# Kernel optimization log

Measured on AMD Instinct MI355X. Metric: run time of the kernel, lower is better.

Reference implementation:

```python
import jax, jax.numpy as jnp
import numpy as np

E = 16        # n_routed_experts
K = 4         # num_experts_per_tok
G = 4         # n_group
TG = 2        # topk_group
NS = 2        # n_shared_experts
H = 1024      # hidden_size
I = 1408      # intermediate_size
SCALE = 1.0   # routed_scaling_factor


def _gate(x2d, gate_w, gate_bias):
    # x2d: [T,H], gate_w: [E,H], gate_bias: [E]
    T = x2d.shape[0]
    logits = x2d.astype(jnp.float32) @ gate_w.astype(jnp.float32).T   # [T,E]
    scores = jax.nn.sigmoid(logits)
    sfc = scores + gate_bias[None, :]
    # group scores = sum of top-2 expert scores within each group
    grp = sfc.reshape(T, G, E // G)
    top2, _ = jax.lax.top_k(grp, 2)
    group_scores = top2.sum(-1)                                       # [T,G]
    _, gidx = jax.lax.top_k(group_scores, TG)                         # [T,TG]
    gmask = jnp.zeros((T, G), sfc.dtype).at[jnp.arange(T)[:, None], gidx].set(1.0)
    smask = jnp.repeat(gmask, E // G, axis=1) > 0                     # [T,E]
    tmp = jnp.where(smask, sfc, 0.0)
    _, topk_idx = jax.lax.top_k(tmp, K)                               # [T,K]
    topk_w = jnp.take_along_axis(scores, topk_idx, axis=1)            # [T,K]
    topk_w = topk_w / (topk_w.sum(-1, keepdims=True) + 1e-20)         # norm_topk_prob
    return topk_idx, topk_w * SCALE


def setup_inputs() -> dict:
    key = jax.random.key(0)
    ks = jax.random.split(key, 8)
    bound = 1.0 / np.sqrt(H)  # kaiming_uniform(a=sqrt(5)) on [E,H]
    return {
        "hidden_states": jax.random.normal(ks[0], (1, 1024, H), jnp.float32),
        "gate_w": jax.random.uniform(ks[1], (E, H), jnp.float32, -bound, bound),
        "gate_bias": jnp.zeros((E,), jnp.float32),
        "gate_proj": jax.random.normal(ks[2], (E, I, H), jnp.float32) * 0.02,
        "up_proj": jax.random.normal(ks[3], (E, I, H), jnp.float32) * 0.02,
        "down_proj": jax.random.normal(ks[4], (E, H, I), jnp.float32) * 0.02,
        "shared_gate_w": jax.random.normal(ks[5], (I * NS, H), jnp.float32) * 0.02,
        "shared_up_w": jax.random.normal(ks[6], (I * NS, H), jnp.float32) * 0.02,
        "shared_down_w": jax.random.normal(ks[7], (H, I * NS), jnp.float32) * 0.02,
    }


def reference(hidden_states, gate_w, gate_bias, gate_proj, up_proj, down_proj,
              shared_gate_w, shared_up_w, shared_down_w):
    orig_shape = hidden_states.shape
    x = hidden_states.reshape(-1, H)                                  # [T,H]
    topk_idx, topk_w = _gate(x, gate_w, gate_bias)
    # per-token per-expert combine weight (top-k indices are unique per token,
    # so scatter-add combine == dense weighted sum)
    combine_w = (jax.nn.one_hot(topk_idx, E, dtype=x.dtype) * topk_w[..., None]).sum(1)  # [T,E]
    g = jnp.einsum('th,eih->tei', x, gate_proj)                       # [T,E,I]
    u = jnp.einsum('th,eih->tei', x, up_proj)
    act = jax.nn.silu(g) * u                                          # SwiGLU
    y = jnp.einsum('tei,ehi,te->th', act, down_proj, combine_w)       # [T,H]
    # shared experts
    sg = x @ shared_gate_w.T
    su = x @ shared_up_w.T
    y = y + (jax.nn.silu(sg) * su) @ shared_down_w.T
    return y.reshape(orig_shape)
```

## Files before the change

### kernel.cpp

```cpp
#include <hip/hip_runtime.h>
#include <hip/hip_bf16.h>

#define T_TOK 1024
#define H_DIM 1024
#define I_DIM 1408
#define NE 16
#define NEP 18
#define BM 256

typedef __attribute__((ext_vector_type(8))) __bf16 bf16x8;
typedef __attribute__((ext_vector_type(4))) float f32x4;

__device__ __forceinline__ bf16x8 cvt8(float4 a, float4 b) {
    bf16x8 r;
    r[0] = (__bf16)a.x; r[1] = (__bf16)a.y; r[2] = (__bf16)a.z; r[3] = (__bf16)a.w;
    r[4] = (__bf16)b.x; r[5] = (__bf16)b.y; r[6] = (__bf16)b.z; r[7] = (__bf16)b.w;
    return r;
}

__device__ __forceinline__ void gll16(const float* g, float* l) {
    __builtin_amdgcn_global_load_lds(
        (const __attribute__((address_space(1))) void*)g,
        (__attribute__((address_space(3))) void*)l, 16, 0, 0);
}

__global__ __launch_bounds__(64) void gate_kernel(
    const float* __restrict__ x, const float* __restrict__ gw,
    const float* __restrict__ gb,
    int* __restrict__ counts, int* __restrict__ etok, float* __restrict__ ew)
{
    const int t = blockIdx.x;
    const int lane = threadIdx.x;
    float s[NE];
#pragma unroll
    for (int e = 0; e < NE; ++e) s[e] = 0.f;
    const float* xr = x + (size_t)t * H_DIM;
    for (int i = lane; i < H_DIM; i += 64) {
        float xv = xr[i];
#pragma unroll
        for (int e = 0; e < NE; ++e) s[e] += xv * gw[e * H_DIM + i];
    }
#pragma unroll
    for (int e = 0; e < NE; ++e) {
        for (int off = 32; off > 0; off >>= 1) s[e] += __shfl_xor(s[e], off);
    }
    if (lane == 0) {
        float scores[NE], sfc[NE];
#pragma unroll
        for (int e = 0; e < NE; ++e) {
            scores[e] = 1.f / (1.f + __expf(-s[e]));
            sfc[e] = scores[e] + gb[e];
        }
        float gsc[4];
#pragma unroll
        for (int g = 0; g < 4; ++g) {
            float m1 = -1e30f, m2 = -1e30f;
#pragma unroll
            for (int j = 0; j < 4; ++j) {
                float v = sfc[4 * g + j];
                if (v > m1) { m2 = m1; m1 = v; } else if (v > m2) { m2 = v; }
            }
            gsc[g] = m1 + m2;
        }
        int g1 = 0;
        for (int g = 1; g < 4; ++g) if (gsc[g] > gsc[g1]) g1 = g;
        int g2 = -1;
        for (int g = 0; g < 4; ++g) {
            if (g == g1) continue;
            if (g2 < 0 || gsc[g] > gsc[g2]) g2 = g;
        }
        float tmp[NE];
#pragma unroll
        for (int e = 0; e < NE; ++e) {
            int gg = e >> 2;
            tmp[e] = (gg == g1 || gg == g2) ? sfc[e] : 0.0f;
        }
        int idxs[4]; float wk[4]; float wsum = 0.f;
#pragma unroll
        for (int k = 0; k < 4; ++k) {
            int bi = 0;
            for (int e = 1; e < NE; ++e) if (tmp[e] > tmp[bi]) bi = e;
            idxs[k] = bi; wk[k] = scores[bi]; wsum += scores[bi];
            tmp[bi] = -1e30f;
        }
        float inv = 1.f / (wsum + 1e-20f);
        for (int k = 0; k < 4; ++k) {
            int e = idxs[k];
            int pos = atomicAdd(&counts[e], 1);
            etok[e * T_TOK + pos] = t;
            ew[e * T_TOK + pos] = wk[k] * inv;
        }
    }
}

__global__ __launch_bounds__(256) void cvtx_kernel(
    const float* __restrict__ x, __hip_bfloat16* __restrict__ x_bf)
{
    int i = (blockIdx.x * 256 + threadIdx.x) * 4;
    float4 v = ((const float4*)x)[i >> 2];
    x_bf[i + 0] = __float2bfloat16(v.x);
    x_bf[i + 1] = __float2bfloat16(v.y);
    x_bf[i + 2] = __float2bfloat16(v.z);
    x_bf[i + 3] = __float2bfloat16(v.w);
}

__global__ __launch_bounds__(256, 2) void gateup_kernel(
    const __hip_bfloat16* __restrict__ x_bf,
    const float* __restrict__ gproj, const float* __restrict__ uproj,
    const float* __restrict__ sgw, const float* __restrict__ suw,
    const int* __restrict__ counts, const int* __restrict__ etok,
    __hip_bfloat16* __restrict__ act, int e0)
{
    const int slot = blockIdx.y;
    const int e = e0 + slot;
    const int cnt = (e < NE) ? counts[e] : T_TOK;
    const int row0 = blockIdx.z * BM;
    if (row0 >= cnt) return;

    __shared__ int toks[BM];
    __shared__ __align__(16) float Bg[3][2048];
    __shared__ __align__(16) float Bu[3][2048];

    const int tid = threadIdx.x;
    {
        int r = row0 + tid;
        toks[tid] = (e < NE) ? ((r < cnt) ? etok[e * T_TOK + r] : 0) : r;
    }

    const int nb0 = blockIdx.x * 64;
    const float *wg, *wu;
    if (e < NE) {
        wg = gproj + (size_t)e * I_DIM * H_DIM;
        wu = uproj + (size_t)e * I_DIM * H_DIM;
    } else {
        wg = sgw + (size_t)(e - NE) * I_DIM * H_DIM;
        wu = suw + (size_t)(e - NE) * I_DIM * H_DIM;
    }

    const int lane = tid & 63;
    const int w = tid >> 6;
    const int col = lane & 15, kq = lane >> 4;

    const int lr8 = lane >> 3;
    const int sgx = (lane & 7) ^ lr8;
    const float* pgW[2]; const float* puW[2];
#pragma unroll
    for (int j = 0; j < 2; ++j) {
        int c = 2 * w + j;
        pgW[j] = wg + (size_t)(nb0 + c * 8 + lr8) * H_DIM + sgx * 4;
        puW[j] = wu + (size_t)(nb0 + c * 8 + lr8) * H_DIM + sgx * 4;
    }
    const int ldsw0 = (2 * w) * 256, ldsw1 = (2 * w + 1) * 256;

    int offs[4][2];
#pragma unroll
    for (int ni = 0; ni < 4; ++ni) {
        int row = ni * 16 + col;
#pragma unroll
        for (int h = 0; h < 2; ++h)
            offs[ni][h] = row * 32 + (((kq * 2 + h) ^ (row & 7)) << 2);
    }

    __syncthreads();

    const __hip_bfloat16* ar[4];
#pragma unroll
    for (int mi = 0; mi < 4; ++mi)
        ar[mi] = x_bf + (size_t)toks[w * 64 + mi * 16 + col] * H_DIM + kq * 8;

    f32x4 accg[4][4], accu[4][4];
#pragma unroll
    for (int mi = 0; mi < 4; ++mi)
#pragma unroll
        for (int ni = 0; ni < 4; ++ni) {
            accg[mi][ni] = (f32x4){0.f, 0.f, 0.f, 0.f};
            accu[mi][ni] = (f32x4){0.f, 0.f, 0.f, 0.f};
        }

    bf16x8 a_cur[4], a_nxt[4];
#pragma unroll
    for (int mi = 0; mi < 4; ++mi) a_cur[mi] = *(const bf16x8*)ar[mi];
    gll16(pgW[0], &Bg[0][ldsw0]); gll16(pgW[1], &Bg[0][ldsw1]);
    gll16(puW[0], &Bu[0][ldsw0]); gll16(puW[1], &Bu[0][ldsw1]);
    gll16(pgW[0] + 32, &Bg[1][ldsw0]); gll16(pgW[1] + 32, &Bg[1][ldsw1]);
    gll16(puW[0] + 32, &Bu[1][ldsw0]); gll16(puW[1] + 32, &Bu[1][ldsw1]);

    int br = 0;
    for (int k = 0; k < 32; ++k) {
        asm volatile("s_waitcnt vmcnt(4)" ::: "memory");
        __builtin_amdgcn_s_barrier();
        __builtin_amdgcn_sched_barrier(0);
        if (k + 1 < 32) {
#pragma unroll
            for (int mi = 0; mi < 4; ++mi)
                a_nxt[mi] = *(const bf16x8*)(ar[mi] + (k + 1) * 32);
        }
        __builtin_amdgcn_sched_barrier(0);
        if (k + 2 < 32) {
            int b2 = br + 2; if (b2 >= 3) b2 -= 3;
            float* bgD = &Bg[0][0] + b2 * 2048;
            float* buD = &Bu[0][0] + b2 * 2048;
            const int ko = (k + 2) * 32;
            gll16(pgW[0] + ko, bgD + ldsw0); gll16(pgW[1] + ko, bgD + ldsw1);
            gll16(puW[0] + ko, buD + ldsw0); gll16(puW[1] + ko, buD + ldsw1);
        }
        __builtin_amdgcn_sched_barrier(0);
        const float* bgR = &Bg[0][0] + br * 2048;
        const float* buR = &Bu[0][0] + br * 2048;
        bf16x8 bg[4], bu[4];
#pragma unroll
        for (int ni = 0; ni < 4; ++ni) {
            float4 lo = *(const float4*)(bgR + offs[ni][0]);
            float4 hi = *(const float4*)(bgR + offs[ni][1]);
            bg[ni] = cvt8(lo, hi);
            float4 lo2 = *(const float4*)(buR + offs[ni][0]);
            float4 hi2 = *(const float4*)(buR + offs[ni][1]);
            bu[ni] = cvt8(lo2, hi2);
        }
#pragma unroll
        for (int mi = 0; mi < 4; ++mi)
#pragma unroll
            for (int ni = 0; ni < 4; ++ni) {
                accg[mi][ni] = __builtin_amdgcn_mfma_f32_16x16x32_bf16(a_cur[mi], bg[ni], accg[mi][ni], 0, 0, 0);
                accu[mi][ni] = __builtin_amdgcn_mfma_f32_16x16x32_bf16(a_cur[mi], bu[ni], accu[mi][ni], 0, 0, 0);
            }
#pragma unroll
        for (int mi = 0; mi < 4; ++mi) a_cur[mi] = a_nxt[mi];
        br += 1; if (br >= 3) br = 0;
    }

#pragma unroll
    for (int mi = 0; mi < 4; ++mi)
#pragma unroll
        for (int ni = 0; ni < 4; ++ni)
#pragma unroll
            for (int r = 0; r < 4; ++r) {
                int lrow = w * 64 + mi * 16 + kq * 4 + r;
                int grow = row0 + lrow;
                float g = accg[mi][ni][r];
                float a = (grow < cnt) ? (g / (1.f + __expf(-g)) * accu[mi][ni][r]) : 0.f;
                act[((size_t)slot * T_TOK + grow) * I_DIM + nb0 + ni * 16 + col] =
                    __float2bfloat16(a);
            }
}

__global__ __launch_bounds__(256, 3) void down_kernel(
    const __hip_bfloat16* __restrict__ act,
    const float* __restrict__ dproj, const float* __restrict__ sdw,
    const int* __restrict__ counts, const int* __restrict__ etok,
    const float* __restrict__ ew, float* __restrict__ y, int e0, int ne)
{
    const int hw = blockIdx.x;
    const int c8 = hw & 7, t = hw >> 3;
    const int nbt = t & 15, gh = t >> 4;
    const int g = c8 + 8 * gh;
    if (g >= ne * 4) return;
    const int slot = g % ne;
    const int z = g / ne;

    const int e = e0 + slot;
    const int cnt = (e < NE) ? counts[e] : T_TOK;
    const int row0 = z * BM;
    if (row0 >= cnt) return;

    __shared__ int toks[BM];
    __shared__ float wts[BM];
    __shared__ __align__(16) float Bd[3][2048];

    const int tid = threadIdx.x;
    {
        int r = row0 + tid;
        if (e < NE) {
            bool ok = r < cnt;
            toks[tid] = ok ? etok[e * T_TOK + r] : 0;
            wts[tid]  = ok ? ew[e * T_TOK + r] : 0.f;
        } else { toks[tid] = r; wts[tid] = 1.f; }
    }

    const int nb0 = nbt * 64;
    const float* wd;
    int wstride;
    if (e < NE) { wd = dproj + (size_t)e * H_DIM * I_DIM; wstride = I_DIM; }
    else        { wd = sdw + (size_t)(e - NE) * I_DIM;    wstride = 2 * I_DIM; }

    const int lane = tid & 63;
    const int w = tid >> 6;
    const int col = lane & 15, kq = lane >> 4;

    const int lr8 = lane >> 3;
    const int sgx = (lane & 7) ^ lr8;
    const float* pdW[2];
#pragma unroll
    for (int j = 0; j < 2; ++j) {
        int c = 2 * w + j;
        pdW[j] = wd + (size_t)(nb0 + c * 8 + lr8) * wstride + sgx * 4;
    }
    const int ldsw0 = (2 * w) * 256, ldsw1 = (2 * w + 1) * 256;

    int offs[4][2];
#pragma unroll
    for (int ni = 0; ni < 4; ++ni) {
        int row = ni * 16 + col;
#pragma unroll
        for (int h = 0; h < 2; ++h)
            offs[ni][h] = row * 32 + (((kq * 2 + h) ^ (row & 7)) << 2);
    }

    __syncthreads();

    const __hip_bfloat16* ar[4];
#pragma unroll
    for (int mi = 0; mi < 4; ++mi)
        ar[mi] = act + ((size_t)slot * T_TOK + row0 + w * 64 + mi * 16 + col) * I_DIM + kq * 8;

    f32x4 acc[4][4];
#pragma unroll
    for (int mi = 0; mi < 4; ++mi)
#pragma unroll
        for (int ni = 0; ni < 4; ++ni) acc[mi][ni] = (f32x4){0.f, 0.f, 0.f, 0.f};

    const int KS = I_DIM / 32;
    bf16x8 a_cur[4], a_nxt[4];
#pragma unroll
    for (int mi = 0; mi < 4; ++mi) a_cur[mi] = *(const bf16x8*)ar[mi];
    gll16(pdW[0], &Bd[0][ldsw0]); gll16(pdW[1], &Bd[0][ldsw1]);
    gll16(pdW[0] + 32, &Bd[1][ldsw0]); gll16(pdW[1] + 32, &Bd[1][ldsw1]);

    int br = 0;
    for (int k = 0; k < KS; ++k) {
        asm volatile("s_waitcnt vmcnt(2)" ::: "memory");
        __builtin_amdgcn_s_barrier();
        __builtin_amdgcn_sched_barrier(0);
        if (k + 1 < KS) {
#pragma unroll
            for (int mi = 0; mi < 4; ++mi)
                a_nxt[mi] = *(const bf16x8*)(ar[mi] + (k + 1) * 32);
        }
        __builtin_amdgcn_sched_barrier(0);
        if (k + 2 < KS) {
            int b2 = br + 2; if (b2 >= 3) b2 -= 3;
            float* bdD = &Bd[0][0] + b2 * 2048;
            const int ko = (k + 2) * 32;
            gll16(pdW[0] + ko, bdD + ldsw0); gll16(pdW[1] + ko, bdD + ldsw1);
        }
        __builtin_amdgcn_sched_barrier(0);
        const float* bdR = &Bd[0][0] + br * 2048;
        bf16x8 b[4];
#pragma unroll
        for (int ni = 0; ni < 4; ++ni) {
            float4 lo = *(const float4*)(bdR + offs[ni][0]);
            float4 hi = *(const float4*)(bdR + offs[ni][1]);
            b[ni] = cvt8(lo, hi);
        }
#pragma unroll
        for (int mi = 0; mi < 4; ++mi)
#pragma unroll
            for (int ni = 0; ni < 4; ++ni)
                acc[mi][ni] = __builtin_amdgcn_mfma_f32_16x16x32_bf16(a_cur[mi], b[ni], acc[mi][ni], 0, 0, 0);
#pragma unroll
        for (int mi = 0; mi < 4; ++mi) a_cur[mi] = a_nxt[mi];
        br += 1; if (br >= 3) br = 0;
    }

#pragma unroll
    for (int mi = 0; mi < 4; ++mi)
#pragma unroll
        for (int ni = 0; ni < 4; ++ni)
#pragma unroll
            for (int r = 0; r < 4; ++r) {
                int lrow = w * 64 + mi * 16 + kq * 4 + r;
                int grow = row0 + lrow;
                if (grow < cnt)
                    atomicAdd(&y[(size_t)toks[lrow] * H_DIM + nb0 + ni * 16 + col],
                              acc[mi][ni][r] * wts[lrow]);
            }
}

extern "C" void kernel_launch(void* const* d_in, const int* in_sizes, int n_in,
                              void* d_out, int out_size, void* d_ws, size_t ws_size,
                              hipStream_t stream) {
    (void)in_sizes; (void)n_in; (void)out_size;
    const float* x  = (const float*)d_in[0];
    const float* gw = (const float*)d_in[1];
    const float* gb = (const float*)d_in[2];
    const float* gp = (const float*)d_in[3];
    const float* up = (const float*)d_in[4];
    const float* dp = (const float*)d_in[5];
    const float* sg = (const float*)d_in[6];
    const float* su = (const float*)d_in[7];
    const float* sd = (const float*)d_in[8];
    float* out = (float*)d_out;

    char* ws = (char*)d_ws;
    int*   counts = (int*)ws;
    int*   etok   = (int*)(ws + 256);
    float* ew     = (float*)(ws + 256 + 65536);
    __hip_bfloat16* x_bf = (__hip_bfloat16*)(ws + 131328);
    __hip_bfloat16* act  = (__hip_bfloat16*)(ws + 2228480);

    size_t fixed = 2228480;
    size_t per_e = (size_t)T_TOK * I_DIM * 2;
    int cap = NEP;
    if (ws_size < fixed + (size_t)NEP * per_e) {
        cap = (ws_size > fixed + per_e) ? (int)((ws_size - fixed) / per_e) : 1;
        if (cap < 1) cap = 1;
    }

    hipMemsetAsync(ws, 0, 256, stream);
    hipMemsetAsync(out, 0, (size_t)T_TOK * H_DIM * 4, stream);

    gate_kernel<<<dim3(T_TOK), dim3(64), 0, stream>>>(x, gw, gb, counts, etok, ew);
    cvtx_kernel<<<dim3(1024), dim3(256), 0, stream>>>(x, x_bf);

    for (int e0 = 0; e0 < NEP; e0 += cap) {
        int ne = NEP - e0 < cap ? NEP - e0 : cap;
        gateup_kernel<<<dim3(I_DIM / 64, ne, T_TOK / BM), dim3(256), 0, stream>>>(
            x_bf, gp, up, sg, su, counts, etok, act, e0);
        int Gp = ((ne * 4 + 7) / 8) * 8;
        down_kernel<<<dim3(16 * Gp), dim3(256), 0, stream>>>(
            act, dp, sd, counts, etok, ew, out, e0, ne);
    }
}
```

Baseline: 488.8 us.

## Double token tile to 512 rows with 8 waves per block; widen gate kernel

The gate-up and down GEMM kernels now process 512 token rows per block with 512 threads (8 waves), and each wave loads one 8-row weight chunk instead of two. Each fp32 weight tile fetched into LDS is therefore reused across twice as many tokens, which roughly halves weight traffic from global memory for the dense-sized experts. The gate kernel also moves to 256 threads with a shared-memory cross-wave reduction. In exchange there are half as many blocks, which may under-fill the GPU for experts with few tokens, and more per-block load-balancing waste when token counts are small.

Measured after the change: 554.8 us. 1.14x slower.

```diff
diff --git a/kernel.cpp b/kernel.cpp
--- a/kernel.cpp
+++ b/kernel.cpp
@@ -6,7 +6,7 @@
 #define I_DIM 1408
 #define NE 16
 #define NEP 18
-#define BM 256
+#define BMG 512
 
 typedef __attribute__((ext_vector_type(8))) __bf16 bf16x8;
 typedef __attribute__((ext_vector_type(4))) float f32x4;
@@ -24,18 +24,23 @@
         (__attribute__((address_space(3))) void*)l, 16, 0, 0);
 }
 
-__global__ __launch_bounds__(64) void gate_kernel(
+__global__ __launch_bounds__(256) void gate_kernel(
     const float* __restrict__ x, const float* __restrict__ gw,
     const float* __restrict__ gb,
     int* __restrict__ counts, int* __restrict__ etok, float* __restrict__ ew)
 {
     const int t = blockIdx.x;
-    const int lane = threadIdx.x;
+    const int tid = threadIdx.x;
+    const int lane = tid & 63, w = tid >> 6;
+    __shared__ float red[4][NE];
+
     float s[NE];
 #pragma unroll
     for (int e = 0; e < NE; ++e) s[e] = 0.f;
     const float* xr = x + (size_t)t * H_DIM;
-    for (int i = lane; i < H_DIM; i += 64) {
+#pragma unroll
+    for (int j = 0; j < 4; ++j) {
+        int i = tid + j * 256;
         float xv = xr[i];
 #pragma unroll
         for (int e = 0; e < NE; ++e) s[e] += xv * gw[e * H_DIM + i];
@@ -45,10 +50,16 @@
         for (int off = 32; off > 0; off >>= 1) s[e] += __shfl_xor(s[e], off);
     }
     if (lane == 0) {
+#pragma unroll
+        for (int e = 0; e < NE; ++e) red[w][e] = s[e];
+    }
+    __syncthreads();
+    if (tid == 0) {
         float scores[NE], sfc[NE];
 #pragma unroll
         for (int e = 0; e < NE; ++e) {
-            scores[e] = 1.f / (1.f + __expf(-s[e]));
+            float lg = red[0][e] + red[1][e] + red[2][e] + red[3][e];
+            scores[e] = 1.f / (1.f + __expf(-lg));
             sfc[e] = scores[e] + gb[e];
         }
         float gsc[4];
@@ -104,7 +115,7 @@
     x_bf[i + 3] = __float2bfloat16(v.w);
 }
 
-__global__ __launch_bounds__(256, 2) void gateup_kernel(
+__global__ __launch_bounds__(512, 2) void gateup_kernel(
     const __hip_bfloat16* __restrict__ x_bf,
     const float* __restrict__ gproj, const float* __restrict__ uproj,
     const float* __restrict__ sgw, const float* __restrict__ suw,
@@ -114,10 +125,10 @@
     const int slot = blockIdx.y;
     const int e = e0 + slot;
     const int cnt = (e < NE) ? counts[e] : T_TOK;
-    const int row0 = blockIdx.z * BM;
+    const int row0 = blockIdx.z * BMG;
     if (row0 >= cnt) return;
 
-    __shared__ int toks[BM];
+    __shared__ int toks[BMG];
     __shared__ __align__(16) float Bg[3][2048];
     __shared__ __align__(16) float Bu[3][2048];
 
@@ -143,14 +154,9 @@
 
     const int lr8 = lane >> 3;
     const int sgx = (lane & 7) ^ lr8;
-    const float* pgW[2]; const float* puW[2];
-#pragma unroll
-    for (int j = 0; j < 2; ++j) {
-        int c = 2 * w + j;
-        pgW[j] = wg + (size_t)(nb0 + c * 8 + lr8) * H_DIM + sgx * 4;
-        puW[j] = wu + (size_t)(nb0 + c * 8 + lr8) * H_DIM + sgx * 4;
-    }
-    const int ldsw0 = (2 * w) * 256, ldsw1 = (2 * w + 1) * 256;
+    const float* pgW = wg + (size_t)(nb0 + w * 8 + lr8) * H_DIM + sgx * 4;
+    const float* puW = wu + (size_t)(nb0 + w * 8 + lr8) * H_DIM + sgx * 4;
+    const int ldsw = w * 256;
 
     int offs[4][2];
 #pragma unroll
@@ -180,14 +186,12 @@
     bf16x8 a_cur[4], a_nxt[4];
 #pragma unroll
     for (int mi = 0; mi < 4; ++mi) a_cur[mi] = *(const bf16x8*)ar[mi];
-    gll16(pgW[0], &Bg[0][ldsw0]); gll16(pgW[1], &Bg[0][ldsw1]);
-    gll16(puW[0], &Bu[0][ldsw0]); gll16(puW[1], &Bu[0][ldsw1]);
-    gll16(pgW[0] + 32, &Bg[1][ldsw0]); gll16(pgW[1] + 32, &Bg[1][ldsw1]);
-    gll16(puW[0] + 32, &Bu[1][ldsw0]); gll16(puW[1] + 32, &Bu[1][ldsw1]);
+    gll16(pgW, &Bg[0][ldsw]); gll16(puW, &Bu[0][ldsw]);
+    gll16(pgW + 32, &Bg[1][ldsw]); gll16(puW + 32, &Bu[1][ldsw]);
 
     int br = 0;
     for (int k = 0; k < 32; ++k) {
-        asm volatile("s_waitcnt vmcnt(4)" ::: "memory");
+        asm volatile("s_waitcnt vmcnt(2)" ::: "memory");
         __builtin_amdgcn_s_barrier();
         __builtin_amdgcn_sched_barrier(0);
         if (k + 1 < 32) {
@@ -198,11 +202,9 @@
         __builtin_amdgcn_sched_barrier(0);
         if (k + 2 < 32) {
             int b2 = br + 2; if (b2 >= 3) b2 -= 3;
-            float* bgD = &Bg[0][0] + b2 * 2048;
-            float* buD = &Bu[0][0] + b2 * 2048;
             const int ko = (k + 2) * 32;
-            gll16(pgW[0] + ko, bgD + ldsw0); gll16(pgW[1] + ko, bgD + ldsw1);
-            gll16(puW[0] + ko, buD + ldsw0); gll16(puW[1] + ko, buD + ldsw1);
+            gll16(pgW + ko, &Bg[0][0] + b2 * 2048 + ldsw);
+            gll16(puW + ko, &Bu[0][0] + b2 * 2048 + ldsw);
         }
         __builtin_amdgcn_sched_barrier(0);
         const float* bgR = &Bg[0][0] + br * 2048;
@@ -244,7 +246,7 @@
             }
 }
 
-__global__ __launch_bounds__(256, 3) void down_kernel(
+__global__ __launch_bounds__(512, 2) void down_kernel(
     const __hip_bfloat16* __restrict__ act,
     const float* __restrict__ dproj, const float* __restrict__ sdw,
     const int* __restrict__ counts, const int* __restrict__ etok,
@@ -254,17 +256,17 @@
     const int c8 = hw & 7, t = hw >> 3;
     const int nbt = t & 15, gh = t >> 4;
     const int g = c8 + 8 * gh;
-    if (g >= ne * 4) return;
+    if (g >= ne * 2) return;
     const int slot = g % ne;
     const int z = g / ne;
 
     const int e = e0 + slot;
     const int cnt = (e < NE) ? counts[e] : T_TOK;
-    const int row0 = z * BM;
+    const int row0 = z * BMG;
     if (row0 >= cnt) return;
 
-    __shared__ int toks[BM];
-    __shared__ float wts[BM];
+    __shared__ int toks[BMG];
+    __shared__ float wts[BMG];
     __shared__ __align__(16) float Bd[3][2048];
 
     const int tid = threadIdx.x;
@@ -289,13 +291,8 @@
 
     const int lr8 = lane >> 3;
     const int sgx = (lane & 7) ^ lr8;
-    const float* pdW[2];
-#pragma unroll
-    for (int j = 0; j < 2; ++j) {
-        int c = 2 * w + j;
-        pdW[j] = wd + (size_t)(nb0 + c * 8 + lr8) * wstride + sgx * 4;
-    }
-    const int ldsw0 = (2 * w) * 256, ldsw1 = (2 * w + 1) * 256;
+    const float* pdW = wd + (size_t)(nb0 + w * 8 + lr8) * wstride + sgx * 4;
+    const int ldsw = w * 256;
 
     int offs[4][2];
 #pragma unroll
@@ -323,12 +320,12 @@
     bf16x8 a_cur[4], a_nxt[4];
 #pragma unroll
     for (int mi = 0; mi < 4; ++mi) a_cur[mi] = *(const bf16x8*)ar[mi];
-    gll16(pdW[0], &Bd[0][ldsw0]); gll16(pdW[1], &Bd[0][ldsw1]);
-    gll16(pdW[0] + 32, &Bd[1][ldsw0]); gll16(pdW[1] + 32, &Bd[1][ldsw1]);
+    gll16(pdW, &Bd[0][ldsw]);
+    gll16(pdW + 32, &Bd[1][ldsw]);
 
     int br = 0;
     for (int k = 0; k < KS; ++k) {
-        asm volatile("s_waitcnt vmcnt(2)" ::: "memory");
+        asm volatile("s_waitcnt vmcnt(1)" ::: "memory");
         __builtin_amdgcn_s_barrier();
         __builtin_amdgcn_sched_barrier(0);
         if (k + 1 < KS) {
@@ -339,9 +336,7 @@
         __builtin_amdgcn_sched_barrier(0);
         if (k + 2 < KS) {
             int b2 = br + 2; if (b2 >= 3) b2 -= 3;
-            float* bdD = &Bd[0][0] + b2 * 2048;
-            const int ko = (k + 2) * 32;
-            gll16(pdW[0] + ko, bdD + ldsw0); gll16(pdW[1] + ko, bdD + ldsw1);
+            gll16(pdW + (k + 2) * 32, &Bd[0][0] + b2 * 2048 + ldsw);
         }
         __builtin_amdgcn_sched_barrier(0);
         const float* bdR = &Bd[0][0] + br * 2048;
@@ -409,15 +404,15 @@
     hipMemsetAsync(ws, 0, 256, stream);
     hipMemsetAsync(out, 0, (size_t)T_TOK * H_DIM * 4, stream);
 
-    gate_kernel<<<dim3(T_TOK), dim3(64), 0, stream>>>(x, gw, gb, counts, etok, ew);
+    gate_kernel<<<dim3(T_TOK), dim3(256), 0, stream>>>(x, gw, gb, counts, etok, ew);
     cvtx_kernel<<<dim3(1024), dim3(256), 0, stream>>>(x, x_bf);
 
     for (int e0 = 0; e0 < NEP; e0 += cap) {
         int ne = NEP - e0 < cap ? NEP - e0 : cap;
-        gateup_kernel<<<dim3(I_DIM / 64, ne, T_TOK / BM), dim3(256), 0, stream>>>(
+        gateup_kernel<<<dim3(I_DIM / 64, ne, T_TOK / BMG), dim3(512), 0, stream>>>(
             x_bf, gp, up, sg, su, counts, etok, act, e0);
-        int Gp = ((ne * 4 + 7) / 8) * 8;
-        down_kernel<<<dim3(16 * Gp), dim3(256), 0, stream>>>(
+        int Gp = ((ne * 2 + 7) / 8) * 8;
+        down_kernel<<<dim3(16 * Gp), dim3(512), 0, stream>>>(
             act, dp, sd, counts, etok, ew, out, e0, ne);
     }
 }
```
